# Kernel optimization log

Measured on AMD Instinct MI355X. Metric: run time of the kernel, lower is better.

## Reference

```python
import jax, jax.numpy as jnp
import numpy as np

B, S, H = 2, 2048, 2048
NQ, NKV, D = 16, 4, 128
GROUPS = NQ // NKV
SCALE = 1.0 / np.sqrt(D).astype(np.float32)


def _make_rope(seq_len, dim, dtype=jnp.float32):
    inv_freq = 1.0 / (10000.0 ** (jnp.arange(0, dim, 2, dtype=jnp.float32) / dim))
    t = jnp.arange(seq_len, dtype=jnp.float32)
    freqs = jnp.outer(t, inv_freq)                      # [S, D/2]
    emb = jnp.concatenate([freqs, freqs], axis=-1)      # [S, D]
    cos = jnp.cos(emb).astype(dtype)[None, :, None, :]  # [1, S, 1, D]
    sin = jnp.sin(emb).astype(dtype)[None, :, None, :]
    return jnp.broadcast_to(cos, (B, seq_len, 1, dim)), jnp.broadcast_to(sin, (B, seq_len, 1, dim))


def _rotate_half(x):
    x1, x2 = jnp.split(x, 2, axis=-1)
    return jnp.concatenate([-x2, x1], axis=-1)


def _apply_rope(x, cos, sin):
    # x: [B, S, Hh, D]; cos/sin: [B, S, 1, D]
    return x * cos + _rotate_half(x) * sin


def setup_inputs() -> dict:
    key = jax.random.key(0)
    ks = jax.random.split(key, 8)
    x = jax.random.normal(ks[0], (B, S, H), dtype=jnp.float32)
    rope_cos, rope_sin = _make_rope(S, D)
    std = 1.0 / np.sqrt(H)
    Wq = jax.random.normal(ks[1], (NQ * D, H), dtype=jnp.float32) * std
    bq = jax.random.normal(ks[2], (NQ * D,), dtype=jnp.float32) * 0.01
    Wk = jax.random.normal(ks[3], (NKV * D, H), dtype=jnp.float32) * std
    bk = jax.random.normal(ks[4], (NKV * D,), dtype=jnp.float32) * 0.01
    Wv = jax.random.normal(ks[5], (NKV * D, H), dtype=jnp.float32) * std
    bv = jax.random.normal(ks[6], (NKV * D,), dtype=jnp.float32) * 0.01
    Wo = jax.random.normal(ks[7], (H, NQ * D), dtype=jnp.float32) * (1.0 / np.sqrt(NQ * D))
    return {"x": x, "rope_cos": rope_cos, "rope_sin": rope_sin,
            "Wq": Wq, "bq": bq, "Wk": Wk, "bk": bk, "Wv": Wv, "bv": bv, "Wo": Wo}


def reference(x, rope_cos, rope_sin, Wq, bq, Wk, bk, Wv, bv, Wo):
    Bx, Sx, _ = x.shape
    q = (x @ Wq.T + bq).reshape(Bx, Sx, NQ, D)
    k = (x @ Wk.T + bk).reshape(Bx, Sx, NKV, D)
    v = (x @ Wv.T + bv).reshape(Bx, Sx, NKV, D)
    q = _apply_rope(q, rope_cos, rope_sin)
    k = _apply_rope(k, rope_cos, rope_sin)
    q = q.transpose(0, 2, 1, 3)   # [B, NQ, S, D]
    k = k.transpose(0, 2, 1, 3)   # [B, NKV, S, D]
    v = v.transpose(0, 2, 1, 3)
    new_k, new_v = k, v           # kv cache (pre-repeat)
    kr = jnp.repeat(k, GROUPS, axis=1)  # [B, NQ, S_k, D]
    vr = jnp.repeat(v, GROUPS, axis=1)
    S_k = kr.shape[2]
    attn = jnp.einsum('bhsd,bhtd->bhst', q, kr) * SCALE
    row = jnp.arange(Sx)[:, None] + (S_k - Sx)
    col = jnp.arange(S_k)[None, :]
    mask = col > row                       # [S, S_k]
    attn = jnp.where(mask[None, None], -jnp.inf, attn)
    attn_max = jnp.max(attn, axis=-1, keepdims=True)
    attn = jnp.exp(attn - attn_max)
    attn = attn / (jnp.sum(attn, axis=-1, keepdims=True) + 1e-9)
    attn = jnp.nan_to_num(attn, nan=0.0)
    out = jnp.einsum('bhst,bhtd->bhsd', attn, vr)
    out = out.transpose(0, 2, 1, 3).reshape(Bx, Sx, NQ * D)
    out = out @ Wo.T
    return (out, new_k, new_v)
```

## Files before the change

kernel.cpp:

```cpp
#include <hip/hip_runtime.h>
#include <cstdint>
#include <cstddef>
#include <math.h>

constexpr int Bc   = 2;
constexpr int Sc   = 2048;
constexpr int Hc   = 2048;
constexpr int NQc  = 16;
constexpr int NKVc = 4;
constexpr int Dc   = 128;
#define SCALE_F 0.08838834764831845f

typedef __attribute__((ext_vector_type(8))) short  bf16x8;
typedef __attribute__((ext_vector_type(4))) float  f32x4;
typedef __attribute__((ext_vector_type(16))) float f32x16;

__device__ __forceinline__ uint16_t f2bf(float f) {
    union { float f; uint32_t u; } v; v.f = f;
    uint32_t u = v.u;
    return (uint16_t)((u + 0x7FFFu + ((u >> 16) & 1u)) >> 16);
}
__device__ __forceinline__ uint32_t pk2bf(float lo, float hi) {
    return (uint32_t)f2bf(lo) | ((uint32_t)f2bf(hi) << 16);
}
__device__ __forceinline__ float bfu2f(uint16_t u) {
    union { uint32_t u; float f; } v; v.u = (uint32_t)u << 16; return v.f;
}
__device__ __forceinline__ void lds_load16(void* lds, const void* g) {
    __builtin_amdgcn_global_load_lds(
        (const __attribute__((address_space(1))) uint32_t*)g,
        (__attribute__((address_space(3))) uint32_t*)lds, 16, 0, 0);
}
__device__ __forceinline__ bf16x8 mk8(uint32_t w0, uint32_t w1, uint32_t w2, uint32_t w3) {
    union { uint32_t u[4]; bf16x8 s; } t;
    t.u[0] = w0; t.u[1] = w1; t.u[2] = w2; t.u[3] = w3; return t.s;
}

__global__ __launch_bounds__(256) void cvt1_kernel(
    const float* __restrict__ x,  const float* __restrict__ wq,
    const float* __restrict__ wk, const float* __restrict__ wv,
    uint16_t* __restrict__ xb, uint16_t* __restrict__ wqkv)
{
    const long long TOT = 3670016LL;
    for (long long i = (long long)blockIdx.x * 256 + threadIdx.x; i < TOT;
         i += (long long)gridDim.x * 256) {
        const float* src; uint16_t* dst; long long off;
        if (i < 2097152LL)      { src = x;  dst = xb;             off = i; }
        else if (i < 3145728LL) { src = wq; dst = wqkv;           off = i - 2097152LL; }
        else if (i < 3407872LL) { src = wk; dst = wqkv + 4194304; off = i - 3145728LL; }
        else                    { src = wv; dst = wqkv + 5242880; off = i - 3407872LL; }
        float4 v = *((const float4*)src + off);
        uint2 o; o.x = pk2bf(v.x, v.y); o.y = pk2bf(v.z, v.w);
        *((uint2*)dst + off) = o;
    }
}

__global__ __launch_bounds__(256) void cvt2_kernel(
    const float* __restrict__ wo, uint16_t* __restrict__ wob)
{
    for (long long i = (long long)blockIdx.x * 256 + threadIdx.x; i < 1048576LL;
         i += (long long)gridDim.x * 256) {
        float4 v = *((const float4*)wo + i);
        uint2 o; o.x = pk2bf(v.x, v.y); o.y = pk2bf(v.z, v.w);
        *((uint2*)wob + i) = o;
    }
}

__device__ __forceinline__ void gemm_stage(const uint16_t* __restrict__ src,
                                           size_t row_stride, uint16_t* lds,
                                           int wid, int lane)
{
    #pragma unroll
    for (int i = 0; i < 4; ++i) {
        const int g = wid * 4 + i;
        const int r = g * 8 + (lane >> 3);
        const int slot = (lane & 7) ^ (r & 7);
        lds_load16(lds + g * 512, src + (size_t)r * row_stride + slot * 8);
    }
}

#define GEMM_CORE(AS, BS, AB, BB)                                              \
    f32x4 acc[4][4] = {};                                                      \
    gemm_stage(AB, 2048, &AS[0][0], wid, lane);                                \
    gemm_stage(BB, 2048, &BS[0][0], wid, lane);                                \
    __syncthreads();                                                           \
    for (int t = 0; t < 32; ++t) {                                             \
        const int cur = t & 1;                                                 \
        if (t + 1 < 32) {                                                      \
            gemm_stage(AB + (t + 1) * 64, 2048, &AS[cur ^ 1][0], wid, lane);   \
            gemm_stage(BB + (t + 1) * 64, 2048, &BS[cur ^ 1][0], wid, lane);   \
        }                                                                      \
        _Pragma("unroll")                                                      \
        for (int kk = 0; kk < 2; ++kk) {                                       \
            bf16x8 av[4], bw[4];                                               \
            _Pragma("unroll")                                                  \
            for (int mi = 0; mi < 4; ++mi) {                                   \
                const int row = wr * 64 + mi * 16 + (lane & 15);               \
                const int slot = (kk * 4 + (lane >> 4)) ^ (row & 7);           \
                av[mi] = *(const bf16x8*)&AS[cur][row * 64 + slot * 8];        \
            }                                                                  \
            _Pragma("unroll")                                                  \
            for (int nj = 0; nj < 4; ++nj) {                                   \
                const int row = wc * 64 + nj * 16 + (lane & 15);               \
                const int slot = (kk * 4 + (lane >> 4)) ^ (row & 7);           \
                bw[nj] = *(const bf16x8*)&BS[cur][row * 64 + slot * 8];        \
            }                                                                  \
            _Pragma("unroll")                                                  \
            for (int mi = 0; mi < 4; ++mi)                                     \
                _Pragma("unroll")                                              \
                for (int nj = 0; nj < 4; ++nj)                                 \
                    acc[mi][nj] = __builtin_amdgcn_mfma_f32_16x16x32_bf16(     \
                        av[mi], bw[nj], acc[mi][nj], 0, 0, 0);                 \
        }                                                                      \
        __syncthreads();                                                       \
    }

__global__ __launch_bounds__(256) void gemm_qkv_kernel(
    const uint16_t* __restrict__ xb, const uint16_t* __restrict__ wqkv,
    const float* __restrict__ bq, const float* __restrict__ bk, const float* __restrict__ bv,
    uint16_t* __restrict__ qb2, float* __restrict__ kbuf, float* __restrict__ vbuf)
{
    __shared__ __align__(16) uint16_t As[2][128 * 64];
    __shared__ __align__(16) uint16_t Bs[2][128 * 64];
    const int tid = threadIdx.x, lane = tid & 63, wid = tid >> 6;
    const int m0 = blockIdx.x * 128, n0 = blockIdx.y * 128;
    const int wr = wid >> 1, wc = wid & 1;
    const uint16_t* Ab = xb + (size_t)m0 * 2048;
    const uint16_t* Bb = wqkv + (size_t)n0 * 2048;

    GEMM_CORE(As, Bs, Ab, Bb)

    const float* bias; int rtype; int nbase;
    if (n0 < 2048)      { bias = bq + n0;          rtype = 0; nbase = n0; }
    else if (n0 < 2560) { bias = bk + (n0 - 2048); rtype = 1; nbase = n0 - 2048; }
    else                { bias = bv + (n0 - 2560); rtype = 2; nbase = n0 - 2560; }
    #pragma unroll
    for (int mi = 0; mi < 4; ++mi) {
        #pragma unroll
        for (int nj = 0; nj < 4; ++nj) {
            const int ct = wc * 64 + nj * 16 + (lane & 15);
            const int nloc = nbase + ct;
            const int head = nloc >> 7, d = nloc & 127;
            const float bval = bias[ct];
            #pragma unroll
            for (int j = 0; j < 4; ++j) {
                const int m = m0 + wr * 64 + mi * 16 + (lane >> 4) * 4 + j;
                const int bb2 = m >> 11, ss = m & 2047;
                const float v = acc[mi][nj][j] + bval;
                if (rtype == 0)
                    qb2[(((size_t)(bb2 * NQc + head) * Sc) + ss) * Dc + d] = f2bf(v);
                else if (rtype == 1)
                    kbuf[(((size_t)(bb2 * NKVc + head) * Sc) + ss) * Dc + d] = v;
                else
                    vbuf[(((size_t)(bb2 * NKVc + head) * Sc) + ss) * Dc + d] = v;
            }
        }
    }
}

__global__ __launch_bounds__(256) void gemm_out_kernel(
    const uint16_t* __restrict__ ab, const uint16_t* __restrict__ wob,
    float* __restrict__ C)
{
    __shared__ __align__(16) uint16_t As[2][128 * 64];
    __shared__ __align__(16) uint16_t Bs[2][128 * 64];
    const int tid = threadIdx.x, lane = tid & 63, wid = tid >> 6;
    const int m0 = blockIdx.x * 128, n0 = blockIdx.y * 128;
    const int wr = wid >> 1, wc = wid & 1;
    const uint16_t* Ab = ab + (size_t)m0 * 2048;
    const uint16_t* Bb = wob + (size_t)n0 * 2048;

    GEMM_CORE(As, Bs, Ab, Bb)

    #pragma unroll
    for (int mi = 0; mi < 4; ++mi) {
        #pragma unroll
        for (int nj = 0; nj < 4; ++nj) {
            const int n = n0 + wc * 64 + nj * 16 + (lane & 15);
            #pragma unroll
            for (int j = 0; j < 4; ++j) {
                const int m = m0 + wr * 64 + mi * 16 + (lane >> 4) * 4 + j;
                C[(size_t)m * 2048 + n] = acc[mi][nj][j];
            }
        }
    }
}

__global__ __launch_bounds__(256) void rope_kernel(
    uint16_t* __restrict__ qb2, float* __restrict__ kbuf,
    const float* __restrict__ cosb, const float* __restrict__ sinb,
    uint16_t* __restrict__ kb2)
{
    const int idx = blockIdx.x * 256 + threadIdx.x;
    const int e = idx & 31;
    int t = idx >> 5;
    const int ss = t & 2047; t >>= 11;
    const int h = t % 20, bb = t / 20;
    const float* cp = cosb + ((size_t)bb * Sc + ss) * Dc;
    const float* sp = sinb + ((size_t)bb * Sc + ss) * Dc;
    const float2 c1 = *(const float2*)(cp + 2 * e);
    const float2 c2 = *(const float2*)(cp + 64 + 2 * e);
    const float2 s1 = *(const float2*)(sp + 2 * e);
    const float2 s2 = *(const float2*)(sp + 64 + 2 * e);
    if (h < NQc) {
        const size_t base = (((size_t)(bb * NQc + h) * Sc) + ss) * Dc;
        const uint32_t u1 = *(const uint32_t*)(qb2 + base + 2 * e);
        const uint32_t u2 = *(const uint32_t*)(qb2 + base + 64 + 2 * e);
        const float x1a = bfu2f((uint16_t)u1), x1b = bfu2f((uint16_t)(u1 >> 16));
        const float x2a = bfu2f((uint16_t)u2), x2b = bfu2f((uint16_t)(u2 >> 16));
        const float lo0 = x1a * c1.x - x2a * s1.x, lo1 = x1b * c1.y - x2b * s1.y;
        const float hi0 = x2a * c2.x + x1a * s2.x, hi1 = x2b * c2.y + x1b * s2.y;
        *(uint32_t*)(qb2 + base + 2 * e)      = pk2bf(lo0, lo1);
        *(uint32_t*)(qb2 + base + 64 + 2 * e) = pk2bf(hi0, hi1);
    } else {
        const int hh = h - NQc;
        const size_t base = (((size_t)(bb * NKVc + hh) * Sc) + ss) * Dc;
        const float2 x1 = *(const float2*)(kbuf + base + 2 * e);
        const float2 x2 = *(const float2*)(kbuf + base + 64 + 2 * e);
        const float lo0 = x1.x * c1.x - x2.x * s1.x, lo1 = x1.y * c1.y - x2.y * s1.y;
        const float hi0 = x2.x * c2.x + x1.x * s2.x, hi1 = x2.y * c2.y + x1.y * s2.y;
        *(float2*)(kbuf + base + 2 * e)      = make_float2(lo0, lo1);
        *(float2*)(kbuf + base + 64 + 2 * e) = make_float2(hi0, hi1);
        *(uint32_t*)(kb2 + base + 2 * e)      = pk2bf(lo0, lo1);
        *(uint32_t*)(kb2 + base + 64 + 2 * e) = pk2bf(hi0, hi1);
    }
}

__global__ __launch_bounds__(256) void vtrans_kernel(
    const float* __restrict__ vbuf, uint16_t* __restrict__ vt)
{
    __shared__ uint16_t T[128][72];
    const int tid = threadIdx.x;
    const int st = blockIdx.x & 31;
    const int bh = blockIdx.x >> 5;
    const float* src = vbuf + ((size_t)bh * Sc + st * 64) * Dc;
    #pragma unroll
    for (int i = 0; i < 8; ++i) {
        const int f = tid + 256 * i;
        const int s_l = f >> 5, d4 = (f & 31) * 4;
        const float4 v = *((const float4*)(src + (size_t)s_l * Dc) + (f & 31));
        T[d4 + 0][s_l] = f2bf(v.x); T[d4 + 1][s_l] = f2bf(v.y);
        T[d4 + 2][s_l] = f2bf(v.z); T[d4 + 3][s_l] = f2bf(v.w);
    }
    __syncthreads();
    uint16_t* dst = vt + (size_t)bh * Dc * Sc + st * 64;
    #pragma unroll
    for (int i = 0; i < 8; ++i) {
        const int g = tid + 256 * i;
        const int d = g >> 4, s4 = (g & 15) * 4;
        *(uint2*)(dst + (size_t)d * Sc + s4) = *(const uint2*)&T[d][s4];
    }
}

__global__ __launch_bounds__(256, 2) void attn_kernel(
    const uint16_t* __restrict__ qb, const uint16_t* __restrict__ kb,
    const uint16_t* __restrict__ vt, uint16_t* __restrict__ ab)
{
    __shared__ __align__(16) uint16_t Ks[2][64 * 128];
    __shared__ __align__(16) uint16_t Vs[2][128 * 64];

    const int tid = threadIdx.x, lane = tid & 63, wid = tid >> 6;
    const int lin = blockIdx.x;
    const int hf = lin >> 8, pp = lin & 255;
    const int qt = hf ? (pp & 15) : (15 - (pp & 15));
    const int bh = (pp >> 4) + hf * 16;
    const int b = bh >> 4, h = bh & 15, hk = h >> 2;
    const int l31 = lane & 31, l5 = lane >> 5;

    const uint16_t* kpB = kb + ((size_t)(b * NKVc + hk) * Sc) * Dc;
    const uint16_t* vpB = vt + ((size_t)(b * NKVc + hk) * Dc) * Sc;

    const uint16_t* qbase =
        qb + (((size_t)(b * NQc + h) * Sc) + qt * 128 + wid * 32 + l31) * Dc;
    bf16x8 qf[8];
    #pragma unroll
    for (int kk = 0; kk < 8; ++kk)
        qf[kk] = *(const bf16x8*)(qbase + kk * 16 + l5 * 8);

    float m_r = -INFINITY, l_r = 0.f;
    f32x16 o0 = {}, o1 = {}, o2 = {}, o3 = {};

    const int qg      = qt * 128 + wid * 32 + l31;
    const int qgw_min = qt * 128 + wid * 32;
    const int qgw_max = qgw_min + 31;
    const int NCH = 2 * qt + 2;
    constexpr float SCL2 = 0.08838834764831845f * 1.4426950408889634f;

    auto stage = [&](int ch, int buf) {
        const int kb0 = ch * 64;
        #pragma unroll
        for (int i = 0; i < 4; ++i) {
            const int g = wid * 4 + i;
            const int row = g * 4 + (lane >> 4);
            const int slot = (lane & 15) ^ (row & 15);
            lds_load16(&Ks[buf][g * 512], kpB + (size_t)(kb0 + row) * Dc + slot * 8);
        }
        #pragma unroll
        for (int i = 0; i < 4; ++i) {
            const int g = wid * 4 + i;
            const int d = g * 8 + (lane >> 3);
            const int slot = (lane & 7) ^ (d & 7);
            lds_load16(&Vs[buf][g * 512], vpB + (size_t)d * Sc + kb0 + slot * 8);
        }
    };

    stage(0, 0);
    __syncthreads();

    for (int ch = 0; ch < NCH; ++ch) {
        const int buf = ch & 1;
        if (ch + 1 < NCH) stage(ch + 1, buf ^ 1);
        const int kb0 = ch * 64;

        if (kb0 <= qgw_max) {
            f32x16 s0 = {}, s1 = {};
            __builtin_amdgcn_s_setprio(1);
            #pragma unroll
            for (int kk = 0; kk < 8; ++kk) {
                const int r0 = l31;
                const int sl0 = (kk * 2 + l5) ^ (r0 & 15);
                const bf16x8 a0 = *(const bf16x8*)&Ks[buf][r0 * 128 + sl0 * 8];
                const int r1 = 32 + l31;
                const int sl1 = (kk * 2 + l5) ^ (r1 & 15);
                const bf16x8 a1 = *(const bf16x8*)&Ks[buf][r1 * 128 + sl1 * 8];
                s0 = __builtin_amdgcn_mfma_f32_32x32x16_bf16(a0, qf[kk], s0, 0, 0, 0);
                s1 = __builtin_amdgcn_mfma_f32_32x32x16_bf16(a1, qf[kk], s1, 0, 0, 0);
            }
            __builtin_amdgcn_s_setprio(0);

            float p[32];
            const bool needmask = (kb0 + 63 > qgw_min);
            #pragma unroll
            for (int r = 0; r < 16; ++r) {
                float v0 = s0[r] * SCL2;
                float v1 = s1[r] * SCL2;
                if (needmask) {
                    const int krel = (r & 3) + 8 * (r >> 2) + 4 * l5;
                    if (kb0 + krel > qg)      v0 = -INFINITY;
                    if (kb0 + 32 + krel > qg) v1 = -INFINITY;
                }
                p[r] = v0; p[16 + r] = v1;
            }
            float tm[16];
            #pragma unroll
            for (int i = 0; i < 16; ++i) tm[i] = fmaxf(p[i], p[16 + i]);
            #pragma unroll
            for (int i = 0; i < 8; ++i) tm[i] = fmaxf(tm[i], tm[8 + i]);
            #pragma unroll
            for (int i = 0; i < 4; ++i) tm[i] = fmaxf(tm[i], tm[4 + i]);
            float rm = fmaxf(fmaxf(tm[0], tm[1]), fmaxf(tm[2], tm[3]));
            rm = fmaxf(rm, __shfl_xor(rm, 32));

            if (!__all(rm <= m_r + 8.0f)) {
                const float mnew = fmaxf(m_r, rm);
                const float alpha = exp2f(m_r - mnew);
                #pragma unroll
                for (int r = 0; r < 16; ++r) {
                    const int qi = (r & 3) + 8 * (r >> 2) + 4 * l5;
                    const float av = __shfl(alpha, qi);
                    o0[r] *= av; o1[r] *= av; o2[r] *= av; o3[r] *= av;
                }
                l_r *= alpha;
                m_r = mnew;
            }

            #pragma unroll
            for (int j = 0; j < 32; ++j) p[j] = exp2f(p[j] - m_r);
            float s8[8];
            #pragma unroll
            for (int i = 0; i < 8; ++i)
                s8[i] = (p[i] + p[8 + i]) + (p[16 + i] + p[24 + i]);
            float sum = ((s8[0] + s8[1]) + (s8[2] + s8[3]))
                      + ((s8[4] + s8[5]) + (s8[6] + s8[7]));
            sum += __shfl_xor(sum, 32);
            l_r += sum;

            uint32_t pb[16];
            #pragma unroll
            for (int j = 0; j < 8; ++j) {
                asm("v_cvt_pk_bf16_f32 %0, %1, %2"
                    : "=v"(pb[j]) : "v"(p[2 * j]), "v"(p[2 * j + 1]));
                asm("v_cvt_pk_bf16_f32 %0, %1, %2"
                    : "=v"(pb[8 + j]) : "v"(p[16 + 2 * j]), "v"(p[16 + 2 * j + 1]));
            }
            #pragma unroll
            for (int g2 = 0; g2 < 4; ++g2) {
                asm("v_permlane32_swap_b32 %0, %1"
                    : "+v"(pb[4 * g2 + 0]), "+v"(pb[4 * g2 + 2]));
                asm("v_permlane32_swap_b32 %0, %1"
                    : "+v"(pb[4 * g2 + 1]), "+v"(pb[4 * g2 + 3]));
            }
            const bf16x8 pa0 = mk8(pb[0],  pb[1],  pb[2],  pb[3]);
            const bf16x8 pa1 = mk8(pb[4],  pb[5],  pb[6],  pb[7]);
            const bf16x8 pa2 = mk8(pb[8],  pb[9],  pb[10], pb[11]);
            const bf16x8 pa3 = mk8(pb[12], pb[13], pb[14], pb[15]);

            __builtin_amdgcn_s_setprio(1);
            #define PV_DV(OO, DV)                                                        \
            {                                                                            \
                const int d = (DV) * 32 + l31;                                           \
                const int rb = d * 64; const int sw = d & 7;                             \
                const bf16x8 b0 = *(const bf16x8*)&Vs[buf][rb + ((0 * 2 + l5) ^ sw) * 8];\
                OO = __builtin_amdgcn_mfma_f32_32x32x16_bf16(pa0, b0, OO, 0, 0, 0);      \
                const bf16x8 b1 = *(const bf16x8*)&Vs[buf][rb + ((1 * 2 + l5) ^ sw) * 8];\
                OO = __builtin_amdgcn_mfma_f32_32x32x16_bf16(pa1, b1, OO, 0, 0, 0);      \
                const bf16x8 b2 = *(const bf16x8*)&Vs[buf][rb + ((2 * 2 + l5) ^ sw) * 8];\
                OO = __builtin_amdgcn_mfma_f32_32x32x16_bf16(pa2, b2, OO, 0, 0, 0);      \
                const bf16x8 b3 = *(const bf16x8*)&Vs[buf][rb + ((3 * 2 + l5) ^ sw) * 8];\
                OO = __builtin_amdgcn_mfma_f32_32x32x16_bf16(pa3, b3, OO, 0, 0, 0);      \
            }
            PV_DV(o0, 0) PV_DV(o1, 1) PV_DV(o2, 2) PV_DV(o3, 3)
            #undef PV_DV
            __builtin_amdgcn_s_setprio(0);
        }

        __syncthreads();
    }

    const float inv = 1.f / (l_r + 1e-9f);
    uint16_t* abase = ab + ((size_t)b * Sc) * 2048 + (size_t)h * Dc;
    #pragma unroll
    for (int r = 0; r < 16; ++r) {
        const int qi = (r & 3) + 8 * (r >> 2) + 4 * l5;
        const float iv = __shfl(inv, qi);
        const int srow = qt * 128 + wid * 32 + qi;
        uint16_t* dst = abase + (size_t)srow * 2048 + l31;
        dst[0]  = f2bf(o0[r] * iv);
        dst[32] = f2bf(o1[r] * iv);
        dst[64] = f2bf(o2[r] * iv);
        dst[96] = f2bf(o3[r] * iv);
    }
}

extern "C" void kernel_launch(void* const* d_in, const int* in_sizes, int n_in,
                              void* d_out, int out_size, void* d_ws, size_t ws_size,
                              hipStream_t stream)
{
    const float* x    = (const float*)d_in[0];
    const float* cosb = (const float*)d_in[1];
    const float* sinb = (const float*)d_in[2];
    const float* Wq   = (const float*)d_in[3];
    const float* bq   = (const float*)d_in[4];
    const float* Wk   = (const float*)d_in[5];
    const float* bk   = (const float*)d_in[6];
    const float* Wv   = (const float*)d_in[7];
    const float* bv   = (const float*)d_in[8];
    const float* Wo   = (const float*)d_in[9];

    float* out  = (float*)d_out;
    float* kout = out  + (size_t)Bc * Sc * Hc;
    float* vout = kout + (size_t)Bc * NKVc * Sc * Dc;
    uint16_t* qb2 = (uint16_t*)out;

    uint8_t* ws = (uint8_t*)d_ws;
    uint16_t* xb   = (uint16_t*)(ws);
    uint16_t* wqkv = (uint16_t*)(ws + (16u << 20));
    uint16_t* kb2  = (uint16_t*)(ws + (16u << 20));
    uint16_t* vb2t = (uint16_t*)(ws + (20u << 20));
    uint16_t* wob  = (uint16_t*)(ws + (24u << 20));
    uint16_t* ab   = (uint16_t*)(ws);

    cvt1_kernel<<<2048, 256, 0, stream>>>(x, Wq, Wk, Wv, xb, wqkv);

    gemm_qkv_kernel<<<dim3(32, 24), 256, 0, stream>>>(xb, wqkv, bq, bk, bv,
                                                      qb2, kout, vout);

    rope_kernel<<<10240, 256, 0, stream>>>(qb2, kout, cosb, sinb, kb2);

    vtrans_kernel<<<256, 256, 0, stream>>>(vout, vb2t);

    cvt2_kernel<<<1024, 256, 0, stream>>>(Wo, wob);

    attn_kernel<<<512, 256, 0, stream>>>(qb2, kb2, vb2t, ab);

    gemm_out_kernel<<<dim3(32, 16), 256, 0, stream>>>(ab, wob, out);
}
```

Baseline: 356.8 us.

## Enlarge GEMM tiles to 256x256 with 512-thread blocks and MFMA priority

Both projection GEMMs move from 128x128 tiles with 4 waves to 256x256 tiles with 8 waves, each wave computing a 128x64 sub-tile. Global-to-LDS staging for A and B is merged into one routine. The loop now syncs with an explicit vmcnt wait plus barrier, and raises wave priority around the MFMA block. The aim is more operand reuse per LDS byte and fewer redundant global loads. The cost is far fewer blocks (192 and 128) than the GPU has CUs, and 128KB of LDS per block, which limits occupancy.

```diff
diff --git a/kernel.cpp b/kernel.cpp
--- a/kernel.cpp
+++ b/kernel.cpp
@@ -66,76 +66,86 @@
     }
 }
 
-__device__ __forceinline__ void gemm_stage(const uint16_t* __restrict__ src,
-                                           size_t row_stride, uint16_t* lds,
-                                           int wid, int lane)
-{
-    #pragma unroll
-    for (int i = 0; i < 4; ++i) {
-        const int g = wid * 4 + i;
-        const int r = g * 8 + (lane >> 3);
-        const int slot = (lane & 7) ^ (r & 7);
-        lds_load16(lds + g * 512, src + (size_t)r * row_stride + slot * 8);
-    }
-}
-
-#define GEMM_CORE(AS, BS, AB, BB)                                              \
-    f32x4 acc[4][4] = {};                                                      \
-    gemm_stage(AB, 2048, &AS[0][0], wid, lane);                                \
-    gemm_stage(BB, 2048, &BS[0][0], wid, lane);                                \
-    __syncthreads();                                                           \
-    for (int t = 0; t < 32; ++t) {                                             \
-        const int cur = t & 1;                                                 \
-        if (t + 1 < 32) {                                                      \
-            gemm_stage(AB + (t + 1) * 64, 2048, &AS[cur ^ 1][0], wid, lane);   \
-            gemm_stage(BB + (t + 1) * 64, 2048, &BS[cur ^ 1][0], wid, lane);   \
-        }                                                                      \
-        _Pragma("unroll")                                                      \
-        for (int kk = 0; kk < 2; ++kk) {                                       \
-            bf16x8 av[4], bw[4];                                               \
-            _Pragma("unroll")                                                  \
-            for (int mi = 0; mi < 4; ++mi) {                                   \
-                const int row = wr * 64 + mi * 16 + (lane & 15);               \
-                const int slot = (kk * 4 + (lane >> 4)) ^ (row & 7);           \
-                av[mi] = *(const bf16x8*)&AS[cur][row * 64 + slot * 8];        \
-            }                                                                  \
-            _Pragma("unroll")                                                  \
-            for (int nj = 0; nj < 4; ++nj) {                                   \
-                const int row = wc * 64 + nj * 16 + (lane & 15);               \
-                const int slot = (kk * 4 + (lane >> 4)) ^ (row & 7);           \
-                bw[nj] = *(const bf16x8*)&BS[cur][row * 64 + slot * 8];        \
-            }                                                                  \
-            _Pragma("unroll")                                                  \
-            for (int mi = 0; mi < 4; ++mi)                                     \
-                _Pragma("unroll")                                              \
-                for (int nj = 0; nj < 4; ++nj)                                 \
-                    acc[mi][nj] = __builtin_amdgcn_mfma_f32_16x16x32_bf16(     \
-                        av[mi], bw[nj], acc[mi][nj], 0, 0, 0);                 \
-        }                                                                      \
-        __syncthreads();                                                       \
-    }
-
-__global__ __launch_bounds__(256) void gemm_qkv_kernel(
+__device__ __forceinline__ void stage256(const uint16_t* __restrict__ Ab,
+                                         const uint16_t* __restrict__ Bb,
+                                         int koff, uint16_t* sA, uint16_t* sB,
+                                         int wid, int lane)
+{
+    #pragma unroll
+    for (int i = 0; i < 8; ++i) {
+        const int g = wid * 8 + i;
+        if (g < 32) {
+            const int r = g * 8 + (lane >> 3);
+            lds_load16(sA + g * 512,
+                       Ab + (size_t)r * 2048 + koff + (((lane & 7) ^ (r & 7)) * 8));
+        } else {
+            const int gb = g - 32;
+            const int r = gb * 8 + (lane >> 3);
+            lds_load16(sB + gb * 512,
+                       Bb + (size_t)r * 2048 + koff + (((lane & 7) ^ (r & 7)) * 8));
+        }
+    }
+}
+
+#define GEMM256_CORE(SA, SB, AB, BB)                                            \
+    f32x4 acc[8][4] = {};                                                       \
+    stage256(AB, BB, 0, &SA[0][0], &SB[0][0], wid, lane);                       \
+    for (int t = 0; t < 32; ++t) {                                              \
+        const int cur = t & 1;                                                  \
+        asm volatile("s_waitcnt vmcnt(0)" ::: "memory");                        \
+        __builtin_amdgcn_sched_barrier(0);                                      \
+        __builtin_amdgcn_s_barrier();                                           \
+        __builtin_amdgcn_sched_barrier(0);                                      \
+        if (t + 1 < 32)                                                         \
+            stage256(AB, BB, (t + 1) * 64, &SA[cur ^ 1][0], &SB[cur ^ 1][0],    \
+                     wid, lane);                                                \
+        _Pragma("unroll")                                                       \
+        for (int kk = 0; kk < 2; ++kk) {                                        \
+            bf16x8 av[8], bw[4];                                                \
+            _Pragma("unroll")                                                   \
+            for (int mi = 0; mi < 8; ++mi) {                                    \
+                const int row = wr * 128 + mi * 16 + (lane & 15);               \
+                const int s = (kk * 4 + (lane >> 4)) ^ (row & 7);               \
+                av[mi] = *(const bf16x8*)&SA[cur][row * 64 + s * 8];            \
+            }                                                                   \
+            _Pragma("unroll")                                                   \
+            for (int nj = 0; nj < 4; ++nj) {                                    \
+                const int row = wc * 64 + nj * 16 + (lane & 15);                \
+                const int s = (kk * 4 + (lane >> 4)) ^ (row & 7);               \
+                bw[nj] = *(const bf16x8*)&SB[cur][row * 64 + s * 8];            \
+            }                                                                   \
+            __builtin_amdgcn_s_setprio(1);                                      \
+            _Pragma("unroll")                                                   \
+            for (int mi = 0; mi < 8; ++mi)                                      \
+                _Pragma("unroll")                                               \
+                for (int nj = 0; nj < 4; ++nj)                                  \
+                    acc[mi][nj] = __builtin_amdgcn_mfma_f32_16x16x32_bf16(      \
+                        av[mi], bw[nj], acc[mi][nj], 0, 0, 0);                  \
+            __builtin_amdgcn_s_setprio(0);                                      \
+        }                                                                       \
+    }
+
+__global__ __launch_bounds__(512, 2) void gemm_qkv_kernel(
     const uint16_t* __restrict__ xb, const uint16_t* __restrict__ wqkv,
     const float* __restrict__ bq, const float* __restrict__ bk, const float* __restrict__ bv,
     uint16_t* __restrict__ qb2, float* __restrict__ kbuf, float* __restrict__ vbuf)
 {
-    __shared__ __align__(16) uint16_t As[2][128 * 64];
-    __shared__ __align__(16) uint16_t Bs[2][128 * 64];
+    __shared__ __align__(16) uint16_t SA[2][256 * 64];
+    __shared__ __align__(16) uint16_t SB[2][256 * 64];
     const int tid = threadIdx.x, lane = tid & 63, wid = tid >> 6;
-    const int m0 = blockIdx.x * 128, n0 = blockIdx.y * 128;
-    const int wr = wid >> 1, wc = wid & 1;
+    const int m0 = blockIdx.x * 256, n0 = blockIdx.y * 256;
+    const int wr = wid >> 2, wc = wid & 3;
     const uint16_t* Ab = xb + (size_t)m0 * 2048;
     const uint16_t* Bb = wqkv + (size_t)n0 * 2048;
 
-    GEMM_CORE(As, Bs, Ab, Bb)
+    GEMM256_CORE(SA, SB, Ab, Bb)
 
     const float* bias; int rtype; int nbase;
     if (n0 < 2048)      { bias = bq + n0;          rtype = 0; nbase = n0; }
     else if (n0 < 2560) { bias = bk + (n0 - 2048); rtype = 1; nbase = n0 - 2048; }
     else                { bias = bv + (n0 - 2560); rtype = 2; nbase = n0 - 2560; }
     #pragma unroll
-    for (int mi = 0; mi < 4; ++mi) {
+    for (int mi = 0; mi < 8; ++mi) {
         #pragma unroll
         for (int nj = 0; nj < 4; ++nj) {
             const int ct = wc * 64 + nj * 16 + (lane & 15);
@@ -144,7 +154,7 @@
             const float bval = bias[ct];
             #pragma unroll
             for (int j = 0; j < 4; ++j) {
-                const int m = m0 + wr * 64 + mi * 16 + (lane >> 4) * 4 + j;
+                const int m = m0 + wr * 128 + mi * 16 + (lane >> 4) * 4 + j;
                 const int bb2 = m >> 11, ss = m & 2047;
                 const float v = acc[mi][nj][j] + bval;
                 if (rtype == 0)
@@ -158,28 +168,28 @@
     }
 }
 
-__global__ __launch_bounds__(256) void gemm_out_kernel(
+__global__ __launch_bounds__(512, 2) void gemm_out_kernel(
     const uint16_t* __restrict__ ab, const uint16_t* __restrict__ wob,
     float* __restrict__ C)
 {
-    __shared__ __align__(16) uint16_t As[2][128 * 64];
-    __shared__ __align__(16) uint16_t Bs[2][128 * 64];
+    __shared__ __align__(16) uint16_t SA[2][256 * 64];
+    __shared__ __align__(16) uint16_t SB[2][256 * 64];
     const int tid = threadIdx.x, lane = tid & 63, wid = tid >> 6;
-    const int m0 = blockIdx.x * 128, n0 = blockIdx.y * 128;
-    const int wr = wid >> 1, wc = wid & 1;
+    const int m0 = blockIdx.x * 256, n0 = blockIdx.y * 256;
+    const int wr = wid >> 2, wc = wid & 3;
     const uint16_t* Ab = ab + (size_t)m0 * 2048;
     const uint16_t* Bb = wob + (size_t)n0 * 2048;
 
-    GEMM_CORE(As, Bs, Ab, Bb)
-
-    #pragma unroll
-    for (int mi = 0; mi < 4; ++mi) {
+    GEMM256_CORE(SA, SB, Ab, Bb)
+
+    #pragma unroll
+    for (int mi = 0; mi < 8; ++mi) {
         #pragma unroll
         for (int nj = 0; nj < 4; ++nj) {
             const int n = n0 + wc * 64 + nj * 16 + (lane & 15);
             #pragma unroll
             for (int j = 0; j < 4; ++j) {
-                const int m = m0 + wr * 64 + mi * 16 + (lane >> 4) * 4 + j;
+                const int m = m0 + wr * 128 + mi * 16 + (lane >> 4) * 4 + j;
                 C[(size_t)m * 2048 + n] = acc[mi][nj][j];
             }
         }
@@ -462,7 +472,7 @@
 
     cvt1_kernel<<<2048, 256, 0, stream>>>(x, Wq, Wk, Wv, xb, wqkv);
 
-    gemm_qkv_kernel<<<dim3(32, 24), 256, 0, stream>>>(xb, wqkv, bq, bk, bv,
+    gemm_qkv_kernel<<<dim3(16, 12), 512, 0, stream>>>(xb, wqkv, bq, bk, bv,
                                                       qb2, kout, vout);
 
     rope_kernel<<<10240, 256, 0, stream>>>(qb2, kout, cosb, sinb, kb2);
@@ -473,5 +483,5 @@
 
     attn_kernel<<<512, 256, 0, stream>>>(qb2, kb2, vb2t, ab);
 
-    gemm_out_kernel<<<dim3(32, 16), 256, 0, stream>>>(ab, wob, out);
-}
+    gemm_out_kernel<<<dim3(16, 8), 512, 0, stream>>>(ab, wob, out);
+}
```

New measurement: 354.7 us. About the same (-0.6%).
